# Performance work log

Hardware: AMD Instinct MI355X
Metric: run time of the kernel (lower is better)

Reference implementation:

```python
import jax, jax.numpy as jnp
import numpy as np
import math

NUM_GRIDS = 128
INPUT_DIM = 128
OUTPUT_DIM = 128
BATCH = 8192
INIT_SCALE = 0.1


def _borders_cdf_grid(n_chunks):
    # inverse Laplace CDF grid borders, exactly as in the torch module
    def inv(u):
        return np.log(2.0 * u) if u <= 0.5 else -np.log(2.0 * (1.0 - u))
    cs = 1.0 / n_chunks
    b = [inv(i * cs) for i in range(1, n_chunks)]
    left = b[0] - (b[1] - b[0])
    right = b[-1] + (b[-1] - b[-2])
    return np.array([left] + b + [right], dtype=np.float32)  # [n_chunks+1]


def setup_inputs() -> dict:
    key = jax.random.key(0)
    kx, kp = jax.random.split(key)
    x = jax.random.normal(kx, (INPUT_DIM, BATCH), dtype=jnp.float32)
    s = INIT_SCALE / math.sqrt(INPUT_DIM)
    func_parameter = jax.random.uniform(
        kp, (NUM_GRIDS + 1, OUTPUT_DIM, INPUT_DIM), dtype=jnp.float32,
        minval=-s, maxval=s)
    borders = jnp.asarray(_borders_cdf_grid(NUM_GRIDS))
    inverse_chunk_lengths = 1.0 / (borders[1:] - borders[:-1])  # [NUM_GRIDS]
    return {"x": x, "func_parameter": func_parameter,
            "borders": borders, "inverse_chunk_lengths": inverse_chunk_lengths}


def reference(x, func_parameter, borders, inverse_chunk_lengths):
    # x: [I, B]; func_parameter: [G+1, O, I]
    G = borders.shape[0] - 1
    I = x.shape[0]
    # Laplace CDF: R -> [0, 1]
    exp_na = jnp.exp(-jnp.abs(x))
    cdf = jnp.where(x > 0, 1.0 - 0.5 * exp_na, 0.5 * exp_na)
    # bucketize on uniform CDF grid (truncation == floor since cdf*G >= 0)
    idx = jnp.clip((cdf * G).astype(jnp.int32), 0, G - 1)        # [I, B]
    idx_next = jnp.clip(idx + 1, 0, G)                           # [I, B]
    left = borders[idx]                                          # [I, B]
    inv_len = inverse_chunk_lengths[idx]                         # [I, B]
    d = (x - left) * inv_len                                     # [I, B]
    # gather per-input-dim parameter rows: val[i, b, o] = P[idx[i,b], o, i]
    Pt = jnp.transpose(func_parameter, (2, 0, 1))                # [I, G+1, O]
    rows = jnp.arange(I)[:, None]                                # [I, 1]
    val_l = Pt[rows, idx]                                        # [I, B, O]
    val_r = Pt[rows, idx_next]                                   # [I, B, O]
    out = ((1.0 - d)[..., None] * val_l + d[..., None] * val_r).sum(axis=0)  # [B, O]
    return out.T                                                 # [O, B]
```

## Files before the change

### kernel.cpp

```cpp
#include <hip/hip_runtime.h>
#include <cstdint>


#define NG 128
#define NI 128
#define NO 128
#define NB 8192

using half2v = __attribute__((ext_vector_type(2))) _Float16;

__device__ inline uint32_t pack_f16x2(float lo, float hi) {
    _Float16 hl = (_Float16)lo, hh = (_Float16)hi;
    return (uint32_t)__builtin_bit_cast(unsigned short, hl) |
           ((uint32_t)__builtin_bit_cast(unsigned short, hh) << 16);
}

__global__ __launch_bounds__(256) void build_q(const float* __restrict__ P,
                                               uint32_t* __restrict__ Q) {
    __shared__ float lp[32][129];
    __shared__ float ln[32][129];
    const int g  = blockIdx.x >> 2;
    const int o0 = (blockIdx.x & 3) * 32;
    const int t  = threadIdx.x;
    #pragma unroll
    for (int p = 0; p < 16; ++p) {
        int e = p * 256 + t;
        int ol = e >> 7, i = e & 127;
        lp[ol][i] = P[(size_t)(g * NO + o0 + ol) * NI + i];
        ln[ol][i] = P[(size_t)((g + 1) * NO + o0 + ol) * NI + i];
    }
    __syncthreads();
    #pragma unroll
    for (int p = 0; p < 16; ++p) {
        int e = p * 256 + t;
        int i = e >> 5, ol = e & 31;
        float pl = lp[ol][i];
        float dd = ln[ol][i] - pl;
        Q[((size_t)i * NG + g) * NO + o0 + ol] = pack_f16x2(pl, dd);
    }
}

__global__ __launch_bounds__(256) void build_t(const float* __restrict__ x,
                                               const float* __restrict__ borders,
                                               const float* __restrict__ icl,
                                               uint32_t* __restrict__ T) {
    const int e0 = (blockIdx.x * 256 + threadIdx.x) * 4;
    const float4 xv = *(const float4*)(x + e0);
    uint32_t r[4];
    const float xs[4] = {xv.x, xv.y, xv.z, xv.w};
    #pragma unroll
    for (int k = 0; k < 4; ++k) {
        float v = xs[k];
        float ea = __expf(-fabsf(v));
        float cdf = v > 0.f ? 1.f - 0.5f * ea : 0.5f * ea;
        int idx = (int)(cdf * 128.f);
        idx = idx > 127 ? 127 : idx;
        float d = (v - borders[idx]) * icl[idx];
        _Float16 hd = (_Float16)d;
        r[k] = (uint32_t)idx |
               ((uint32_t)__builtin_bit_cast(unsigned short, hd) << 16);
    }
    *(uint4*)(T + e0) = make_uint4(r[0], r[1], r[2], r[3]);
}

__global__ __launch_bounds__(512) void main_k(const uint32_t* __restrict__ Q,
                                              const uint32_t* __restrict__ T,
                                              float* __restrict__ out) {
    __shared__ float sout[16][132];
    const int t    = threadIdx.x;
    const int wv   = t >> 6;
    const int lane = t & 63;
    const int bblk = blockIdx.x * 16;
    const int b0   = __builtin_amdgcn_readfirstlane(bblk + wv * 2);
    const bool hi  = lane >= 32;
    const uint32_t laneoff = (uint32_t)((lane & 31) * 16);

    const char* Qb = (const char*)Q;
    float a0 = 0.f, a1 = 0.f, a2 = 0.f, a3 = 0.f;
    #pragma unroll 8
    for (int i = 0; i < NI; ++i) {
        uint64_t tt = *(const uint64_t*)(T + (size_t)i * NB + b0);
        uint32_t t0 = (uint32_t)tt;
        uint32_t t1 = (uint32_t)(tt >> 32);
        uint32_t w0 = (t0 & 0xFFFF0000u) | 0x3C00u;
        uint32_t w1 = (t1 & 0xFFFF0000u) | 0x3C00u;
        uint32_t q0 = (t0 & 127u) << 9;
        uint32_t q1 = (t1 & 127u) << 9;
        uint32_t wb  = hi ? w1 : w0;
        uint32_t off = (uint32_t)(i << 16) + (hi ? q1 : q0) + laneoff;
        uint4 q = *(const uint4*)(Qb + off);
        half2v w2 = __builtin_bit_cast(half2v, wb);
        a0 = __builtin_amdgcn_fdot2(__builtin_bit_cast(half2v, q.x), w2, a0, false);
        a1 = __builtin_amdgcn_fdot2(__builtin_bit_cast(half2v, q.y), w2, a1, false);
        a2 = __builtin_amdgcn_fdot2(__builtin_bit_cast(half2v, q.z), w2, a2, false);
        a3 = __builtin_amdgcn_fdot2(__builtin_bit_cast(half2v, q.w), w2, a3, false);
    }
    {
        int r = wv * 2 + (hi ? 1 : 0);
        int c = (lane & 31) * 4;
        *(float4*)&sout[r][c] = make_float4(a0, a1, a2, a3);
    }
    __syncthreads();
    {
        int o  = t >> 2;
        int bq = t & 3;
        float4 v = make_float4(sout[bq * 4 + 0][o], sout[bq * 4 + 1][o],
                               sout[bq * 4 + 2][o], sout[bq * 4 + 3][o]);
        __builtin_nontemporal_store(v.x, &out[(size_t)o * NB + bblk + bq * 4 + 0]);
        __builtin_nontemporal_store(v.y, &out[(size_t)o * NB + bblk + bq * 4 + 1]);
        __builtin_nontemporal_store(v.z, &out[(size_t)o * NB + bblk + bq * 4 + 2]);
        __builtin_nontemporal_store(v.w, &out[(size_t)o * NB + bblk + bq * 4 + 3]);
    }
}

extern "C" void kernel_launch(void* const* d_in, const int* in_sizes, int n_in,
                              void* d_out, int out_size, void* d_ws, size_t ws_size,
                              hipStream_t stream) {
    const float* x       = (const float*)d_in[0];
    const float* P       = (const float*)d_in[1];
    const float* borders = (const float*)d_in[2];
    const float* icl     = (const float*)d_in[3];
    float* out = (float*)d_out;

    uint32_t* Q = (uint32_t*)d_ws;
    uint32_t* T = Q + (size_t)NI * NG * NO;

    hipLaunchKernelGGL(build_q, dim3(NG * 4), dim3(256), 0, stream, P, Q);
    hipLaunchKernelGGL(build_t, dim3(NI * NB / 1024), dim3(256), 0, stream,
                       x, borders, icl, T);
    hipLaunchKernelGGL(main_k, dim3(NB / 16), dim3(512), 0, stream, Q, T, out);
}
```

Measured before the change: 100.7 us.

## Split input dimension across XCD-mapped slices with partial-sum reduction kernel

The main kernel now splits the 128 input dims into 4 slices of 32. Block indices are mapped so each XCD handles a single slice, which keeps only a quarter of the Q table (8 MB of 32 MB) hot in that XCD's L2 and should cut gather misses. Each slice writes partial sums to a workspace buffer, and a new reduce kernel adds the four partials into the output. The cost is 4x more partial-output traffic (about 16 MB written and re-read), plus an extra launch.

Measured after the change: 102.3 us. Within noise of the previous version (+1.6%).

```diff
diff --git a/kernel.cpp b/kernel.cpp
--- a/kernel.cpp
+++ b/kernel.cpp
@@ -6,8 +6,11 @@
 #define NI 128
 #define NO 128
 #define NB 8192
+#define NSL 4
+#define ISL 32
 
-using half2v = __attribute__((ext_vector_type(2))) _Float16;
+using half2v  = __attribute__((ext_vector_type(2))) _Float16;
+using float4v = __attribute__((ext_vector_type(4))) float;
 
 __device__ inline uint32_t pack_f16x2(float lo, float hi) {
     _Float16 hl = (_Float16)lo, hh = (_Float16)hi;
@@ -65,20 +68,25 @@
 
 __global__ __launch_bounds__(512) void main_k(const uint32_t* __restrict__ Q,
                                               const uint32_t* __restrict__ T,
-                                              float* __restrict__ out) {
+                                              float* __restrict__ part) {
     __shared__ float sout[16][132];
-    const int t    = threadIdx.x;
-    const int wv   = t >> 6;
-    const int lane = t & 63;
-    const int bblk = blockIdx.x * 16;
-    const int b0   = __builtin_amdgcn_readfirstlane(bblk + wv * 2);
-    const bool hi  = lane >= 32;
+    const int t     = threadIdx.x;
+    const int wv    = t >> 6;
+    const int lane  = t & 63;
+    const int bx    = blockIdx.x;
+    const int xcd   = bx & 7;
+    const int slice = xcd & 3;
+    const int jb    = (bx >> 3) * 2 + ((xcd >> 2) & 1);
+    const int bblk  = jb * 16;
+    const int i0    = slice * ISL;
+    const int b0    = __builtin_amdgcn_readfirstlane(bblk + wv * 2);
+    const bool hi   = lane >= 32;
     const uint32_t laneoff = (uint32_t)((lane & 31) * 16);
 
     const char* Qb = (const char*)Q;
     float a0 = 0.f, a1 = 0.f, a2 = 0.f, a3 = 0.f;
     #pragma unroll 8
-    for (int i = 0; i < NI; ++i) {
+    for (int i = i0; i < i0 + ISL; ++i) {
         uint64_t tt = *(const uint64_t*)(T + (size_t)i * NB + b0);
         uint32_t t0 = (uint32_t)tt;
         uint32_t t1 = (uint32_t)(tt >> 32);
@@ -101,16 +109,28 @@
         *(float4*)&sout[r][c] = make_float4(a0, a1, a2, a3);
     }
     __syncthreads();
+    float* ps = part + (size_t)slice * NO * NB;
     {
         int o  = t >> 2;
         int bq = t & 3;
-        float4 v = make_float4(sout[bq * 4 + 0][o], sout[bq * 4 + 1][o],
-                               sout[bq * 4 + 2][o], sout[bq * 4 + 3][o]);
-        __builtin_nontemporal_store(v.x, &out[(size_t)o * NB + bblk + bq * 4 + 0]);
-        __builtin_nontemporal_store(v.y, &out[(size_t)o * NB + bblk + bq * 4 + 1]);
-        __builtin_nontemporal_store(v.z, &out[(size_t)o * NB + bblk + bq * 4 + 2]);
-        __builtin_nontemporal_store(v.w, &out[(size_t)o * NB + bblk + bq * 4 + 3]);
+        size_t base = (size_t)o * NB + bblk + bq * 4;
+        __builtin_nontemporal_store(sout[bq * 4 + 0][o], &ps[base + 0]);
+        __builtin_nontemporal_store(sout[bq * 4 + 1][o], &ps[base + 1]);
+        __builtin_nontemporal_store(sout[bq * 4 + 2][o], &ps[base + 2]);
+        __builtin_nontemporal_store(sout[bq * 4 + 3][o], &ps[base + 3]);
     }
+}
+
+__global__ __launch_bounds__(256) void reduce_k(const float* __restrict__ part,
+                                                float* __restrict__ out) {
+    const size_t f = ((size_t)blockIdx.x * 256 + threadIdx.x) * 4;
+    const size_t S = (size_t)NO * NB;
+    float4v a = __builtin_nontemporal_load((const float4v*)(part + f));
+    float4v b = __builtin_nontemporal_load((const float4v*)(part + f + S));
+    float4v c = __builtin_nontemporal_load((const float4v*)(part + f + 2 * S));
+    float4v d = __builtin_nontemporal_load((const float4v*)(part + f + 3 * S));
+    float4v r = a + b + c + d;
+    __builtin_nontemporal_store(r, (float4v*)(out + f));
 }
 
 extern "C" void kernel_launch(void* const* d_in, const int* in_sizes, int n_in,
@@ -122,11 +142,15 @@
     const float* icl     = (const float*)d_in[3];
     float* out = (float*)d_out;
 
-    uint32_t* Q = (uint32_t*)d_ws;
-    uint32_t* T = Q + (size_t)NI * NG * NO;
+    uint32_t* Q    = (uint32_t*)d_ws;
+    uint32_t* T    = Q + (size_t)NI * NG * NO;
+    float*    part = (float*)(T + (size_t)NI * NB);
 
     hipLaunchKernelGGL(build_q, dim3(NG * 4), dim3(256), 0, stream, P, Q);
     hipLaunchKernelGGL(build_t, dim3(NI * NB / 1024), dim3(256), 0, stream,
                        x, borders, icl, T);
-    hipLaunchKernelGGL(main_k, dim3(NB / 16), dim3(512), 0, stream, Q, T, out);
+    hipLaunchKernelGGL(main_k, dim3(NB / 16 * NSL), dim3(512), 0, stream,
+                       Q, T, part);
+    hipLaunchKernelGGL(reduce_k, dim3(NO * NB / 1024), dim3(256), 0, stream,
+                       part, out);
 }
```

## Stage per-output-slice parameter tables in LDS with double-buffered async loads

Applied to the files above, without the earlier changes.

Reorganizes the packed parameter table so each block owns a 4-output slice and stages that slice's rows for 8 input dims at a time into shared memory through global_load_lds. The next phase's rows are fetched while the current one computes. Each thread now handles one batch element and reads its table entry from LDS instead of scattered global/L2 reads. The trade-off is that every block rereads the full T index array, 32 times in total across output slices, and pays a block-wide barrier per phase.

Result: no change. 101.0 us (+0.3%).

```diff
diff --git a/kernel.cpp b/kernel.cpp
--- a/kernel.cpp
+++ b/kernel.cpp
@@ -6,6 +6,9 @@
 #define NI 128
 #define NO 128
 #define NB 8192
+#define WO 4
+#define PH 8
+#define NPH (NI / PH)
 
 using half2v = __attribute__((ext_vector_type(2))) _Float16;
 
@@ -16,7 +19,7 @@
 }
 
 __global__ __launch_bounds__(256) void build_q(const float* __restrict__ P,
-                                               uint32_t* __restrict__ Q) {
+                                               uint32_t* __restrict__ Q2) {
     __shared__ float lp[32][129];
     __shared__ float ln[32][129];
     const int g  = blockIdx.x >> 2;
@@ -31,12 +34,19 @@
     }
     __syncthreads();
     #pragma unroll
-    for (int p = 0; p < 16; ++p) {
+    for (int p = 0; p < 4; ++p) {
         int e = p * 256 + t;
-        int i = e >> 5, ol = e & 31;
-        float pl = lp[ol][i];
-        float dd = ln[ol][i] - pl;
-        Q[((size_t)i * NG + g) * NO + o0 + ol] = pack_f16x2(pl, dd);
+        int sl = e >> 7, i = e & 127;
+        uint32_t r[4];
+        #pragma unroll
+        for (int ow = 0; ow < 4; ++ow) {
+            float pl = lp[sl * 4 + ow][i];
+            float dd = ln[sl * 4 + ow][i] - pl;
+            r[ow] = pack_f16x2(pl, dd);
+        }
+        int s = (o0 >> 2) + sl;
+        *(uint4*)(Q2 + ((size_t)(s * NI + i) * NG + g) * 4) =
+            make_uint4(r[0], r[1], r[2], r[3]);
     }
 }
 
@@ -63,54 +73,64 @@
     *(uint4*)(T + e0) = make_uint4(r[0], r[1], r[2], r[3]);
 }
 
-__global__ __launch_bounds__(512) void main_k(const uint32_t* __restrict__ Q,
-                                              const uint32_t* __restrict__ T,
-                                              float* __restrict__ out) {
-    __shared__ float sout[16][132];
+__global__ __launch_bounds__(1024) void main_k(const uint32_t* __restrict__ Q2,
+                                               const uint32_t* __restrict__ T,
+                                               float* __restrict__ out) {
+    __shared__ uint32_t slab[2][PH][NG * WO];
     const int t    = threadIdx.x;
     const int wv   = t >> 6;
     const int lane = t & 63;
-    const int bblk = blockIdx.x * 16;
-    const int b0   = __builtin_amdgcn_readfirstlane(bblk + wv * 2);
-    const bool hi  = lane >= 32;
-    const uint32_t laneoff = (uint32_t)((lane & 31) * 16);
+    const int bx   = blockIdx.x;
+    const int s    = bx & 31;
+    const int bblk = (bx >> 5) << 10;
+    const int bme  = bblk + (wv << 6) + lane;
+    const uint32_t* Qs = Q2 + (size_t)s * NI * NG * WO;
+    const int st_il = wv >> 1;
+    const int st_k  = ((wv & 1) << 8) + (lane << 2);
 
-    const char* Qb = (const char*)Q;
     float a0 = 0.f, a1 = 0.f, a2 = 0.f, a3 = 0.f;
-    #pragma unroll 8
-    for (int i = 0; i < NI; ++i) {
-        uint64_t tt = *(const uint64_t*)(T + (size_t)i * NB + b0);
-        uint32_t t0 = (uint32_t)tt;
-        uint32_t t1 = (uint32_t)(tt >> 32);
-        uint32_t w0 = (t0 & 0xFFFF0000u) | 0x3C00u;
-        uint32_t w1 = (t1 & 0xFFFF0000u) | 0x3C00u;
-        uint32_t q0 = (t0 & 127u) << 9;
-        uint32_t q1 = (t1 & 127u) << 9;
-        uint32_t wb  = hi ? w1 : w0;
-        uint32_t off = (uint32_t)(i << 16) + (hi ? q1 : q0) + laneoff;
-        uint4 q = *(const uint4*)(Qb + off);
-        half2v w2 = __builtin_bit_cast(half2v, wb);
-        a0 = __builtin_amdgcn_fdot2(__builtin_bit_cast(half2v, q.x), w2, a0, false);
-        a1 = __builtin_amdgcn_fdot2(__builtin_bit_cast(half2v, q.y), w2, a1, false);
-        a2 = __builtin_amdgcn_fdot2(__builtin_bit_cast(half2v, q.z), w2, a2, false);
-        a3 = __builtin_amdgcn_fdot2(__builtin_bit_cast(half2v, q.w), w2, a3, false);
-    }
+
     {
-        int r = wv * 2 + (hi ? 1 : 0);
-        int c = (lane & 31) * 4;
-        *(float4*)&sout[r][c] = make_float4(a0, a1, a2, a3);
+        const uint32_t* src = Qs + (size_t)st_il * (NG * WO) + st_k;
+        __builtin_amdgcn_global_load_lds(
+            (const __attribute__((address_space(1))) uint32_t*)src,
+            (__attribute__((address_space(3))) uint32_t*)&slab[0][st_il][st_k],
+            16, 0, 0);
     }
     __syncthreads();
-    {
-        int o  = t >> 2;
-        int bq = t & 3;
-        float4 v = make_float4(sout[bq * 4 + 0][o], sout[bq * 4 + 1][o],
-                               sout[bq * 4 + 2][o], sout[bq * 4 + 3][o]);
-        __builtin_nontemporal_store(v.x, &out[(size_t)o * NB + bblk + bq * 4 + 0]);
-        __builtin_nontemporal_store(v.y, &out[(size_t)o * NB + bblk + bq * 4 + 1]);
-        __builtin_nontemporal_store(v.z, &out[(size_t)o * NB + bblk + bq * 4 + 2]);
-        __builtin_nontemporal_store(v.w, &out[(size_t)o * NB + bblk + bq * 4 + 3]);
+
+    for (int p = 0; p < NPH; ++p) {
+        const int cur = p & 1;
+        if (p < NPH - 1) {
+            const uint32_t* src =
+                Qs + (size_t)((p + 1) * PH + st_il) * (NG * WO) + st_k;
+            __builtin_amdgcn_global_load_lds(
+                (const __attribute__((address_space(1))) uint32_t*)src,
+                (__attribute__((address_space(3))) uint32_t*)
+                    &slab[cur ^ 1][st_il][st_k],
+                16, 0, 0);
+        }
+        const uint32_t* Trow = T + (size_t)p * PH * NB + bme;
+        #pragma unroll
+        for (int il = 0; il < PH; ++il) {
+            uint32_t tw  = Trow[(size_t)il * NB];
+            uint32_t w2b = (tw & 0xFFFF0000u) | 0x3C00u;
+            uint32_t off = (tw & 127u) << 2;
+            uint4 q = *(const uint4*)&slab[cur][il][off];
+            half2v w2 = __builtin_bit_cast(half2v, w2b);
+            a0 = __builtin_amdgcn_fdot2(__builtin_bit_cast(half2v, q.x), w2, a0, false);
+            a1 = __builtin_amdgcn_fdot2(__builtin_bit_cast(half2v, q.y), w2, a1, false);
+            a2 = __builtin_amdgcn_fdot2(__builtin_bit_cast(half2v, q.z), w2, a2, false);
+            a3 = __builtin_amdgcn_fdot2(__builtin_bit_cast(half2v, q.w), w2, a3, false);
+        }
+        __syncthreads();
     }
+
+    size_t ob = (size_t)(s * 4) * NB + bme;
+    __builtin_nontemporal_store(a0, out + ob);
+    __builtin_nontemporal_store(a1, out + ob + NB);
+    __builtin_nontemporal_store(a2, out + ob + 2 * (size_t)NB);
+    __builtin_nontemporal_store(a3, out + ob + 3 * (size_t)NB);
 }
 
 extern "C" void kernel_launch(void* const* d_in, const int* in_sizes, int n_in,
@@ -122,11 +142,12 @@
     const float* icl     = (const float*)d_in[3];
     float* out = (float*)d_out;
 
-    uint32_t* Q = (uint32_t*)d_ws;
-    uint32_t* T = Q + (size_t)NI * NG * NO;
+    uint32_t* Q2 = (uint32_t*)d_ws;
+    uint32_t* T  = Q2 + (size_t)NO * NI * NG;
 
-    hipLaunchKernelGGL(build_q, dim3(NG * 4), dim3(256), 0, stream, P, Q);
+    hipLaunchKernelGGL(build_q, dim3(NG * 4), dim3(256), 0, stream, P, Q2);
     hipLaunchKernelGGL(build_t, dim3(NI * NB / 1024), dim3(256), 0, stream,
                        x, borders, icl, T);
-    hipLaunchKernelGGL(main_k, dim3(NB / 16), dim3(512), 0, stream, Q, T, out);
+    hipLaunchKernelGGL(main_k, dim3((NB / 1024) * 32), dim3(1024), 0, stream,
+                       Q2, T, out);
 }
```
